# Kernel optimization log

Measured on AMD Instinct MI355X. Metric: run time of the kernel, lower is better.

Reference implementation:

```python
import jax, jax.numpy as jnp
import numpy as np

N = 50000          # nodes
E = 1600000        # edges (avg degree 32)
B = 64             # graphs in batch
IN_CH = 128
HEADS = 8
HD = 8             # head_dim = ceil(64/8)
GH = HEADS * HD    # 64 = gat_hidden_dim
HIDDEN = 64
NC = 10
NEG_SLOPE = 0.2
BN_EPS = 1e-5
SIGMA = 0.5


def setup_inputs() -> dict:
    key = jax.random.key(0)
    ks = jax.random.split(key, 24)
    s = 0.1
    inp = {
        "x": jax.random.normal(ks[0], (N, IN_CH), jnp.float32),
        "raw_x": jax.random.uniform(ks[1], (N, 3), jnp.float32),
        "edge_index": jax.random.randint(ks[2], (2, E), 0, N, jnp.int32),
        "batch": jnp.sort(jax.random.randint(ks[3], (N,), 0, B, jnp.int32)),
        # conv1 (heads=8, out=8, edge_dim=1)
        "W1": jax.random.normal(ks[4], (IN_CH, GH), jnp.float32) * s,
        "att_src1": jax.random.normal(ks[5], (HEADS, HD), jnp.float32) * s,
        "att_dst1": jax.random.normal(ks[6], (HEADS, HD), jnp.float32) * s,
        "We1": jax.random.normal(ks[7], (1, GH), jnp.float32) * s,
        "att_e1": jax.random.normal(ks[8], (HEADS, HD), jnp.float32) * s,
        "b1": jax.random.normal(ks[9], (GH,), jnp.float32) * s,
        "gamma1": jnp.ones((GH,), jnp.float32),
        "beta1": jnp.zeros((GH,), jnp.float32),
        "rm1": jax.random.normal(ks[10], (GH,), jnp.float32) * s,
        "rv1": jax.random.uniform(ks[11], (GH,), jnp.float32) + 0.5,
        # conv2 (heads=1, out=64, edge_dim=1)
        "W2": jax.random.normal(ks[12], (GH, HIDDEN), jnp.float32) * s,
        "att_src2": jax.random.normal(ks[13], (1, HIDDEN), jnp.float32) * s,
        "att_dst2": jax.random.normal(ks[14], (1, HIDDEN), jnp.float32) * s,
        "We2": jax.random.normal(ks[15], (1, HIDDEN), jnp.float32) * s,
        "att_e2": jax.random.normal(ks[16], (1, HIDDEN), jnp.float32) * s,
        "b2": jax.random.normal(ks[17], (HIDDEN,), jnp.float32) * s,
        "gamma2": jnp.ones((HIDDEN,), jnp.float32),
        "beta2": jnp.zeros((HIDDEN,), jnp.float32),
        "rm2": jax.random.normal(ks[18], (HIDDEN,), jnp.float32) * s,
        "rv2": jax.random.uniform(ks[19], (HIDDEN,), jnp.float32) + 0.5,
        # classifier
        "Wc": jax.random.normal(ks[20], (HIDDEN, NC), jnp.float32) * s,
        "bc": jax.random.normal(ks[21], (NC,), jnp.float32) * s,
    }
    return inp


def _gat_conv(x, src, dst, edge_attr, W, a_src, a_dst, W_e, a_e, bias, heads, out_ch, n):
    """PyG GATConv (concat=True, add_self_loops=True, fill_value='mean', eval mode)."""
    e0 = edge_attr.shape[0]
    # self-loop edge_attr = mean of incoming edge_attr per node (0 if isolated)
    cnt = jax.ops.segment_sum(jnp.ones((e0,), x.dtype), dst, num_segments=n)
    loop_attr = jax.ops.segment_sum(edge_attr, dst, num_segments=n) / jnp.maximum(cnt, 1.0)[:, None]
    loops = jnp.arange(n, dtype=src.dtype)
    src2 = jnp.concatenate([src, loops])
    dst2 = jnp.concatenate([dst, loops])
    ea = jnp.concatenate([edge_attr, loop_attr], axis=0)          # [E2, 1]
    h = (x @ W).reshape(n, heads, out_ch)                          # [N, H, D]
    al_s = (h * a_src).sum(-1)                                     # [N, H]
    al_d = (h * a_dst).sum(-1)                                     # [N, H]
    al_e = ((ea @ W_e).reshape(-1, heads, out_ch) * a_e).sum(-1)   # [E2, H]
    logits = al_s[src2] + al_d[dst2] + al_e                        # [E2, H]
    logits = jnp.where(logits >= 0, logits, NEG_SLOPE * logits)    # leaky_relu
    # segment softmax over destination nodes (every node has a self loop)
    m = jax.ops.segment_max(logits, dst2, num_segments=n)
    ex = jnp.exp(logits - m[dst2])
    alpha = ex / jax.ops.segment_sum(ex, dst2, num_segments=n)[dst2]
    out = jax.ops.segment_sum(h[src2] * alpha[:, :, None], dst2, num_segments=n)
    return out.reshape(n, heads * out_ch) + bias


def _bn_eval(x, gamma, beta, rm, rv):
    return (x - rm) * (gamma / jnp.sqrt(rv + BN_EPS)) + beta


def reference(x, raw_x, edge_index, batch,
              W1, att_src1, att_dst1, We1, att_e1, b1, gamma1, beta1, rm1, rv1,
              W2, att_src2, att_dst2, We2, att_e2, b2, gamma2, beta2, rm2, rv2,
              Wc, bc):
    src, dst = edge_index[0], edge_index[1]
    # gaussian edge weights from raw features
    diff = raw_x[src] - raw_x[dst]
    dist2 = (diff * diff).sum(axis=1)
    edge_w = jnp.exp(-dist2 / (2.0 * SIGMA * SIGMA))[:, None]      # [E, 1]
    # eval mode: dropout is identity
    h = _gat_conv(x, src, dst, edge_w, W1, att_src1, att_dst1, We1, att_e1, b1, HEADS, HD, N)
    h = jax.nn.elu(_bn_eval(h, gamma1, beta1, rm1, rv1))
    h = _gat_conv(h, src, dst, edge_w, W2, att_src2, att_dst2, We2, att_e2, b2, 1, HIDDEN, N)
    h = jax.nn.elu(_bn_eval(h, gamma2, beta2, rm2, rv2))
    # global mean pool over graphs
    cnt = jax.ops.segment_sum(jnp.ones((N,), h.dtype), batch, num_segments=B)
    g = jax.ops.segment_sum(h, batch, num_segments=B) / jnp.maximum(cnt, 1.0)[:, None]
    return g @ Wc + bc
```

## Files before the change

kernel.cpp:

```cpp
#include <hip/hip_runtime.h>
#include <math.h>

#define N_NODES 50000
#define N_EDGES 1600000
#define NBATCH  64
#define INCH    128
#define HEADS   8
#define HD      8
#define GH      64
#define HIDDEN  64
#define NC      10
#define NEG_SLOPE 0.2f
#define BN_EPS  1e-5f

#define SCAN_TPB 1024
#define NTILES   ((N_NODES + SCAN_TPB - 1) / SCAN_TPB)

__global__ __launch_bounds__(256) void edge_kernel(
    const int* __restrict__ ei, const float* __restrict__ raw,
    float* __restrict__ ea, float* __restrict__ easum, int* __restrict__ cnt) {
  int e = blockIdx.x * blockDim.x + threadIdx.x;
  if (e >= N_EDGES) return;
  int s = ei[e], d = ei[N_EDGES + e];
  float dx = raw[s*3+0] - raw[d*3+0];
  float dy = raw[s*3+1] - raw[d*3+1];
  float dz = raw[s*3+2] - raw[d*3+2];
  float w = __expf(-2.0f * (dx*dx + dy*dy + dz*dz));
  ea[e] = w;
  atomicAdd(&easum[d], w);
  atomicAdd(&cnt[d], 1);
}

__global__ __launch_bounds__(SCAN_TPB) void scan_part(
    const int* __restrict__ cnt, const float* __restrict__ easum,
    int* __restrict__ rowptr, float* __restrict__ loopat, int* __restrict__ bsum) {
  __shared__ int s[SCAN_TPB];
  int t = threadIdx.x;
  int i = blockIdx.x * SCAN_TPB + t;
  int v = (i < N_NODES) ? cnt[i] : 0;
  s[t] = v; __syncthreads();
  for (int off = 1; off < SCAN_TPB; off <<= 1) {
    int u = (t >= off) ? s[t - off] : 0;
    __syncthreads();
    s[t] += u;
    __syncthreads();
  }
  if (i < N_NODES) {
    rowptr[i] = s[t] - v;
    loopat[i] = easum[i] / fmaxf((float)v, 1.0f);
  }
  if (t == SCAN_TPB - 1) bsum[blockIdx.x] = s[t];
}

__global__ __launch_bounds__(64) void scan_top(int* __restrict__ bsum, int* __restrict__ rowptr) {
  int t = threadIdx.x;
  int v = (t < NTILES) ? bsum[t] : 0;
  int orig = v;
  for (int off = 1; off < 64; off <<= 1) {
    int u = __shfl_up(v, off);
    if (t >= off) v += u;
  }
  if (t < NTILES) bsum[t] = v - orig;
  if (t == 0) rowptr[N_NODES] = N_EDGES;
}

__global__ __launch_bounds__(SCAN_TPB) void scan_add(int* __restrict__ rowptr, const int* __restrict__ bsum) {
  int i = blockIdx.x * SCAN_TPB + threadIdx.x;
  if (i < N_NODES) rowptr[i] += bsum[blockIdx.x];
}

__global__ __launch_bounds__(256) void scatter_kernel(
    const int* __restrict__ ei, const float* __restrict__ ea,
    const int* __restrict__ rowptr, int* __restrict__ cnt2,
    int* __restrict__ csr_src, float* __restrict__ csr_ea) {
  int e = blockIdx.x * blockDim.x + threadIdx.x;
  if (e >= N_EDGES) return;
  int s = ei[e], d = ei[N_EDGES + e];
  int pos = rowptr[d] + atomicAdd(&cnt2[d], 1);
  csr_src[pos] = s;
  csr_ea[pos] = ea[e];
}

__global__ __launch_bounds__(256) void gemm1_kernel(
    const float* __restrict__ x, const float* __restrict__ W1,
    const float* __restrict__ asrc, const float* __restrict__ adst,
    float* __restrict__ h1, float* __restrict__ als, float* __restrict__ ald) {
  __shared__ float w[INCH * GH];
  for (int i = threadIdx.x; i < INCH * GH / 4; i += blockDim.x)
    ((float4*)w)[i] = ((const float4*)W1)[i];
  __syncthreads();
  int lane = threadIdx.x & 63;
  int waveG = __builtin_amdgcn_readfirstlane((blockIdx.x * blockDim.x + threadIdx.x) >> 6);
  int nWaves = (gridDim.x * blockDim.x) >> 6;
  float a_s = asrc[lane];
  float a_d = adst[lane];
  for (int base = waveG * 4; base < N_NODES; base += nWaves * 4) {
    float acc[4] = {0.f, 0.f, 0.f, 0.f};
    #pragma unroll 8
    for (int k = 0; k < INCH; ++k) {
      float wv = w[k * GH + lane];
      #pragma unroll
      for (int j = 0; j < 4; ++j)
        acc[j] = fmaf(x[(size_t)(base + j) * INCH + k], wv, acc[j]);
    }
    #pragma unroll
    for (int j = 0; j < 4; ++j) {
      int n = base + j;
      float hv = acc[j];
      h1[(size_t)n * GH + lane] = hv;
      float ps = hv * a_s, pd = hv * a_d;
      ps += __shfl_xor(ps, 1); ps += __shfl_xor(ps, 2); ps += __shfl_xor(ps, 4);
      pd += __shfl_xor(pd, 1); pd += __shfl_xor(pd, 2); pd += __shfl_xor(pd, 4);
      if ((lane & 7) == 0) {
        als[n * HEADS + (lane >> 3)] = ps;
        ald[n * HEADS + (lane >> 3)] = pd;
      }
    }
  }
}

__global__ __launch_bounds__(256) void conv1_kernel(
    const float* __restrict__ h1, const float* __restrict__ als,
    const float* __restrict__ ald, const float* __restrict__ We,
    const float* __restrict__ ae, const int* __restrict__ rowptr,
    const int* __restrict__ csr_src, const float* __restrict__ csr_ea,
    const float* __restrict__ loopat, const float* __restrict__ bias,
    const float* __restrict__ gamma, const float* __restrict__ beta,
    const float* __restrict__ rm, const float* __restrict__ rv,
    float* __restrict__ h2) {
  int lane = threadIdx.x & 63;
  int n = blockIdx.x * 4 + (threadIdx.x >> 6);
  if (n >= N_NODES) return;
  int h = lane >> 3;
  float ce = 0.f;
  #pragma unroll
  for (int d = 0; d < HD; ++d) ce = fmaf(We[h * HD + d], ae[h * HD + d], ce);
  float aldn = ald[n * HEADS + h];
  int jb = rowptr[n], je = rowptr[n + 1];
  float m = -1e30f, ssum = 0.f, acc = 0.f;
  for (int j = jb; j < je; ++j) {
    int src = csr_src[j];
    float eaj = csr_ea[j];
    float lg = als[src * HEADS + h] + aldn + eaj * ce;
    lg = (lg >= 0.f) ? lg : NEG_SLOPE * lg;
    float hv = h1[(size_t)src * GH + lane];
    float nm = fmaxf(m, lg);
    float r = __expf(m - nm);
    float p = __expf(lg - nm);
    ssum = ssum * r + p;
    acc  = acc  * r + p * hv;
    m = nm;
  }
  {
    float eaj = loopat[n];
    float lg = als[n * HEADS + h] + aldn + eaj * ce;
    lg = (lg >= 0.f) ? lg : NEG_SLOPE * lg;
    float hv = h1[(size_t)n * GH + lane];
    float nm = fmaxf(m, lg);
    float r = __expf(m - nm);
    float p = __expf(lg - nm);
    ssum = ssum * r + p;
    acc  = acc  * r + p * hv;
  }
  float outv = acc / ssum + bias[lane];
  outv = (outv - rm[lane]) * (gamma[lane] * rsqrtf(rv[lane] + BN_EPS)) + beta[lane];
  outv = (outv > 0.f) ? outv : expm1f(outv);
  h2[(size_t)n * GH + lane] = outv;
}

__global__ __launch_bounds__(256) void gemm2_kernel(
    const float* __restrict__ x, const float* __restrict__ W2,
    const float* __restrict__ asrc, const float* __restrict__ adst,
    float* __restrict__ h2m, float* __restrict__ als, float* __restrict__ ald) {
  __shared__ float w[HIDDEN * HIDDEN];
  for (int i = threadIdx.x; i < HIDDEN * HIDDEN / 4; i += blockDim.x)
    ((float4*)w)[i] = ((const float4*)W2)[i];
  __syncthreads();
  int lane = threadIdx.x & 63;
  int waveG = __builtin_amdgcn_readfirstlane((blockIdx.x * blockDim.x + threadIdx.x) >> 6);
  int nWaves = (gridDim.x * blockDim.x) >> 6;
  float a_s = asrc[lane];
  float a_d = adst[lane];
  for (int base = waveG * 4; base < N_NODES; base += nWaves * 4) {
    float acc[4] = {0.f, 0.f, 0.f, 0.f};
    #pragma unroll 8
    for (int k = 0; k < HIDDEN; ++k) {
      float wv = w[k * HIDDEN + lane];
      #pragma unroll
      for (int j = 0; j < 4; ++j)
        acc[j] = fmaf(x[(size_t)(base + j) * HIDDEN + k], wv, acc[j]);
    }
    #pragma unroll
    for (int j = 0; j < 4; ++j) {
      int n = base + j;
      float hv = acc[j];
      h2m[(size_t)n * HIDDEN + lane] = hv;
      float ps = hv * a_s, pd = hv * a_d;
      #pragma unroll
      for (int off = 1; off < 64; off <<= 1) {
        ps += __shfl_xor(ps, off);
        pd += __shfl_xor(pd, off);
      }
      if (lane == 0) { als[n] = ps; ald[n] = pd; }
    }
  }
}

__global__ __launch_bounds__(256) void conv2_kernel(
    const float* __restrict__ h2m, const float* __restrict__ als,
    const float* __restrict__ ald, const float* __restrict__ We,
    const float* __restrict__ ae, const int* __restrict__ rowptr,
    const int* __restrict__ csr_src, const float* __restrict__ csr_ea,
    const float* __restrict__ loopat, const float* __restrict__ bias,
    const float* __restrict__ gamma, const float* __restrict__ beta,
    const float* __restrict__ rm, const float* __restrict__ rv,
    const int* __restrict__ batch,
    float* __restrict__ pool, int* __restrict__ cntg) {
  int lane = threadIdx.x & 63;
  int n = blockIdx.x * 4 + (threadIdx.x >> 6);
  if (n >= N_NODES) return;
  float ce = We[lane] * ae[lane];
  #pragma unroll
  for (int off = 1; off < 64; off <<= 1) ce += __shfl_xor(ce, off);
  float aldn = ald[n];
  int jb = rowptr[n], je = rowptr[n + 1];
  float m = -1e30f, ssum = 0.f, acc = 0.f;
  for (int j = jb; j < je; ++j) {
    int src = csr_src[j];
    float eaj = csr_ea[j];
    float lg = als[src] + aldn + eaj * ce;
    lg = (lg >= 0.f) ? lg : NEG_SLOPE * lg;
    float hv = h2m[(size_t)src * HIDDEN + lane];
    float nm = fmaxf(m, lg);
    float r = __expf(m - nm);
    float p = __expf(lg - nm);
    ssum = ssum * r + p;
    acc  = acc  * r + p * hv;
    m = nm;
  }
  {
    float eaj = loopat[n];
    float lg = als[n] + aldn + eaj * ce;
    lg = (lg >= 0.f) ? lg : NEG_SLOPE * lg;
    float hv = h2m[(size_t)n * HIDDEN + lane];
    float nm = fmaxf(m, lg);
    float r = __expf(m - nm);
    float p = __expf(lg - nm);
    ssum = ssum * r + p;
    acc  = acc  * r + p * hv;
  }
  float outv = acc / ssum + bias[lane];
  outv = (outv - rm[lane]) * (gamma[lane] * rsqrtf(rv[lane] + BN_EPS)) + beta[lane];
  outv = (outv > 0.f) ? outv : expm1f(outv);
  int b = batch[n];
  atomicAdd(&pool[b * HIDDEN + lane], outv);
  if (lane == 0) atomicAdd(&cntg[b], 1);
}

__global__ __launch_bounds__(640) void final_kernel(
    const float* __restrict__ pool, const int* __restrict__ cntg,
    const float* __restrict__ Wc, const float* __restrict__ bc,
    float* __restrict__ out) {
  int t = threadIdx.x;
  if (t >= NBATCH * NC) return;
  int b = t / NC, c = t - b * NC;
  float inv = 1.0f / fmaxf((float)cntg[b], 1.0f);
  float s = bc[c];
  #pragma unroll
  for (int d = 0; d < HIDDEN; ++d)
    s = fmaf(pool[b * HIDDEN + d] * inv, Wc[d * NC + c], s);
  out[t] = s;
}

extern "C" void kernel_launch(void* const* d_in, const int* in_sizes, int n_in,
                              void* d_out, int out_size, void* d_ws, size_t ws_size,
                              hipStream_t stream) {
  const float* x     = (const float*)d_in[0];
  const float* raw   = (const float*)d_in[1];
  const int*   ei    = (const int*)  d_in[2];
  const int*   batch = (const int*)  d_in[3];
  const float* W1    = (const float*)d_in[4];
  const float* asrc1 = (const float*)d_in[5];
  const float* adst1 = (const float*)d_in[6];
  const float* We1   = (const float*)d_in[7];
  const float* ae1   = (const float*)d_in[8];
  const float* b1    = (const float*)d_in[9];
  const float* g1    = (const float*)d_in[10];
  const float* be1   = (const float*)d_in[11];
  const float* rm1   = (const float*)d_in[12];
  const float* rv1   = (const float*)d_in[13];
  const float* W2    = (const float*)d_in[14];
  const float* asrc2 = (const float*)d_in[15];
  const float* adst2 = (const float*)d_in[16];
  const float* We2   = (const float*)d_in[17];
  const float* ae2   = (const float*)d_in[18];
  const float* b2    = (const float*)d_in[19];
  const float* g2    = (const float*)d_in[20];
  const float* be2   = (const float*)d_in[21];
  const float* rm2   = (const float*)d_in[22];
  const float* rv2   = (const float*)d_in[23];
  const float* Wc    = (const float*)d_in[24];
  const float* bc    = (const float*)d_in[25];
  float* out = (float*)d_out;

  char* ws = (char*)d_ws;
  size_t off = 0;
  auto alloc = [&](size_t bytes) -> void* {
    void* p = ws + off;
    off += bytes;
    off = (off + 255) & ~(size_t)255;
    return p;
  };
  float* ea      = (float*)alloc((size_t)N_EDGES * 4);
  float* csr_ea  = (float*)alloc((size_t)N_EDGES * 4);
  int*   csr_src = (int*)  alloc((size_t)N_EDGES * 4);
  float* easum   = (float*)alloc((size_t)N_NODES * 4);
  int*   cnt     = (int*)  alloc((size_t)N_NODES * 4);
  int*   cnt2    = (int*)  alloc((size_t)N_NODES * 4);
  int*   rowptr  = (int*)  alloc((size_t)(N_NODES + 1) * 4);
  float* loopat  = (float*)alloc((size_t)N_NODES * 4);
  float* h1      = (float*)alloc((size_t)N_NODES * GH * 4);
  float* als1    = (float*)alloc((size_t)N_NODES * HEADS * 4);
  float* ald1    = (float*)alloc((size_t)N_NODES * HEADS * 4);
  float* h2      = (float*)alloc((size_t)N_NODES * GH * 4);
  float* h2m     = (float*)alloc((size_t)N_NODES * HIDDEN * 4);
  float* als2    = (float*)alloc((size_t)N_NODES * 4);
  float* ald2    = (float*)alloc((size_t)N_NODES * 4);
  int*   bsum    = (int*)  alloc(64 * 4);
  float* pool    = (float*)alloc((size_t)NBATCH * HIDDEN * 4);
  int*   cntg    = (int*)  alloc((size_t)NBATCH * 4);

  hipMemsetAsync(easum, 0, (size_t)N_NODES * 4, stream);
  hipMemsetAsync(cnt,   0, (size_t)N_NODES * 4, stream);
  hipMemsetAsync(cnt2,  0, (size_t)N_NODES * 4, stream);
  hipMemsetAsync(pool,  0, (size_t)NBATCH * HIDDEN * 4, stream);
  hipMemsetAsync(cntg,  0, (size_t)NBATCH * 4, stream);

  int egrid = (N_EDGES + 255) / 256;
  edge_kernel<<<egrid, 256, 0, stream>>>(ei, raw, ea, easum, cnt);
  scan_part<<<NTILES, SCAN_TPB, 0, stream>>>(cnt, easum, rowptr, loopat, bsum);
  scan_top<<<1, 64, 0, stream>>>(bsum, rowptr);
  scan_add<<<NTILES, SCAN_TPB, 0, stream>>>(rowptr, bsum);
  scatter_kernel<<<egrid, 256, 0, stream>>>(ei, ea, rowptr, cnt2, csr_src, csr_ea);

  gemm1_kernel<<<1024, 256, 0, stream>>>(x, W1, asrc1, adst1, h1, als1, ald1);
  conv1_kernel<<<(N_NODES + 3) / 4, 256, 0, stream>>>(h1, als1, ald1, We1, ae1,
      rowptr, csr_src, csr_ea, loopat, b1, g1, be1, rm1, rv1, h2);
  gemm2_kernel<<<1024, 256, 0, stream>>>(h2, W2, asrc2, adst2, h2m, als2, ald2);
  conv2_kernel<<<(N_NODES + 3) / 4, 256, 0, stream>>>(h2m, als2, ald2, We2, ae2,
      rowptr, csr_src, csr_ea, loopat, b2, g2, be2, rm2, rv2, batch, pool, cntg);
  final_kernel<<<1, 640, 0, stream>>>(pool, cntg, Wc, bc, out);
}
```

Before: 1.067 ms.

## Chunk GAT aggregation: parallel edge logits/softmax per 64-edge chunk, unrolled gathers

Both GAT convolution kernels now process incoming edges in chunks of 64. Source indices and edge attributes are loaded cooperatively across the wave and staged in LDS. Attention logits and the chunk max and sum are computed in parallel with wave shuffles, replacing the per-edge serial online softmax. The feature gather-accumulate is then unrolled by four so several independent row loads are in flight, which removes serial exp and rescale dependencies and scalar index loads per edge. The cost is extra LDS traffic, shuffles and per-chunk padding work for low-degree nodes.

```diff
diff --git a/kernel.cpp b/kernel.cpp
--- a/kernel.cpp
+++ b/kernel.cpp
@@ -128,41 +128,94 @@
     const float* __restrict__ gamma, const float* __restrict__ beta,
     const float* __restrict__ rm, const float* __restrict__ rv,
     float* __restrict__ h2) {
+  __shared__ int   src_lds[4][64];
+  __shared__ float ea_lds[4][64];
+  __shared__ float ex_lds[4][512];
   int lane = threadIdx.x & 63;
-  int n = blockIdx.x * 4 + (threadIdx.x >> 6);
+  int w = threadIdx.x >> 6;
+  int n = blockIdx.x * 4 + w;
   if (n >= N_NODES) return;
-  int h = lane >> 3;
-  float ce = 0.f;
+  int hA = lane & 7;
+  int e8 = lane >> 3;
+  int hB = lane >> 3;
+  float ceA = 0.f;
   #pragma unroll
-  for (int d = 0; d < HD; ++d) ce = fmaf(We[h * HD + d], ae[h * HD + d], ce);
-  float aldn = ald[n * HEADS + h];
+  for (int d = 0; d < HD; ++d) ceA = fmaf(We[hA * HD + d], ae[hA * HD + d], ceA);
+  float aldnA = ald[n * HEADS + hA];
   int jb = rowptr[n], je = rowptr[n + 1];
-  float m = -1e30f, ssum = 0.f, acc = 0.f;
-  for (int j = jb; j < je; ++j) {
-    int src = csr_src[j];
-    float eaj = csr_ea[j];
-    float lg = als[src * HEADS + h] + aldn + eaj * ce;
+  float m = -1e30f, ssum = 0.f;
+  float acc = 0.f;
+  for (int cb = jb; cb < je; cb += 64) {
+    int cnt = je - cb; if (cnt > 64) cnt = 64;
+    int idx = cb + lane;
+    bool vld = lane < cnt;
+    src_lds[w][lane] = vld ? csr_src[idx] : 0;
+    ea_lds[w][lane]  = vld ? csr_ea[idx] : 0.f;
+    float lg[8];
+    #pragma unroll
+    for (int sub = 0; sub < 8; ++sub) {
+      int eo = sub * 8 + e8;
+      int s = src_lds[w][eo];
+      float l = als[s * HEADS + hA] + aldnA + ea_lds[w][eo] * ceA;
+      l = (l >= 0.f) ? l : NEG_SLOPE * l;
+      lg[sub] = (eo < cnt) ? l : -1e30f;
+    }
+    float cm = lg[0];
+    #pragma unroll
+    for (int sub = 1; sub < 8; ++sub) cm = fmaxf(cm, lg[sub]);
+    cm = fmaxf(cm, __shfl_xor(cm, 8));
+    cm = fmaxf(cm, __shfl_xor(cm, 16));
+    cm = fmaxf(cm, __shfl_xor(cm, 32));
+    float nm = fmaxf(m, cm);
+    float sc = __expf(m - nm);
+    float csum = 0.f;
+    #pragma unroll
+    for (int sub = 0; sub < 8; ++sub) {
+      float ex = __expf(lg[sub] - nm);
+      csum += ex;
+      ex_lds[w][sub * 64 + lane] = ex;
+    }
+    csum += __shfl_xor(csum, 8);
+    csum += __shfl_xor(csum, 16);
+    csum += __shfl_xor(csum, 32);
+    ssum = ssum * sc + csum;
+    m = nm;
+    float scB = __shfl(sc, hB);
+    acc *= scB;
+    int j = 0;
+    for (; j + 3 < cnt; j += 4) {
+      int s0 = src_lds[w][j],   s1 = src_lds[w][j+1];
+      int s2 = src_lds[w][j+2], s3 = src_lds[w][j+3];
+      float x0 = ex_lds[w][(j  )*8 + hB], x1 = ex_lds[w][(j+1)*8 + hB];
+      float x2 = ex_lds[w][(j+2)*8 + hB], x3 = ex_lds[w][(j+3)*8 + hB];
+      float v0 = h1[(size_t)s0 * GH + lane];
+      float v1 = h1[(size_t)s1 * GH + lane];
+      float v2 = h1[(size_t)s2 * GH + lane];
+      float v3 = h1[(size_t)s3 * GH + lane];
+      acc = fmaf(x0, v0, acc); acc = fmaf(x1, v1, acc);
+      acc = fmaf(x2, v2, acc); acc = fmaf(x3, v3, acc);
+    }
+    for (; j < cnt; ++j) {
+      int s0 = src_lds[w][j];
+      float x0 = ex_lds[w][j*8 + hB];
+      acc = fmaf(x0, h1[(size_t)s0 * GH + lane], acc);
+    }
+  }
+  float mB = __shfl(m, hB);
+  float sB = __shfl(ssum, hB);
+  float ceB = 0.f;
+  #pragma unroll
+  for (int d = 0; d < HD; ++d) ceB = fmaf(We[hB * HD + d], ae[hB * HD + d], ceB);
+  {
+    float lg = als[n * HEADS + hB] + ald[n * HEADS + hB] + loopat[n] * ceB;
     lg = (lg >= 0.f) ? lg : NEG_SLOPE * lg;
-    float hv = h1[(size_t)src * GH + lane];
-    float nm = fmaxf(m, lg);
-    float r = __expf(m - nm);
+    float nm = fmaxf(mB, lg);
+    float r = __expf(mB - nm);
     float p = __expf(lg - nm);
-    ssum = ssum * r + p;
-    acc  = acc  * r + p * hv;
-    m = nm;
-  }
-  {
-    float eaj = loopat[n];
-    float lg = als[n * HEADS + h] + aldn + eaj * ce;
-    lg = (lg >= 0.f) ? lg : NEG_SLOPE * lg;
-    float hv = h1[(size_t)n * GH + lane];
-    float nm = fmaxf(m, lg);
-    float r = __expf(m - nm);
-    float p = __expf(lg - nm);
-    ssum = ssum * r + p;
-    acc  = acc  * r + p * hv;
-  }
-  float outv = acc / ssum + bias[lane];
+    sB = sB * r + p;
+    acc = acc * r + p * h1[(size_t)n * GH + lane];
+  }
+  float outv = acc / sB + bias[lane];
   outv = (outv - rm[lane]) * (gamma[lane] * rsqrtf(rv[lane] + BN_EPS)) + beta[lane];
   outv = (outv > 0.f) ? outv : expm1f(outv);
   h2[(size_t)n * GH + lane] = outv;
@@ -216,8 +269,11 @@
     const float* __restrict__ rm, const float* __restrict__ rv,
     const int* __restrict__ batch,
     float* __restrict__ pool, int* __restrict__ cntg) {
+  __shared__ int   src_lds[4][64];
+  __shared__ float ex_lds[4][64];
   int lane = threadIdx.x & 63;
-  int n = blockIdx.x * 4 + (threadIdx.x >> 6);
+  int w = threadIdx.x >> 6;
+  int n = blockIdx.x * 4 + w;
   if (n >= N_NODES) return;
   float ce = We[lane] * ae[lane];
   #pragma unroll
@@ -225,29 +281,56 @@
   float aldn = ald[n];
   int jb = rowptr[n], je = rowptr[n + 1];
   float m = -1e30f, ssum = 0.f, acc = 0.f;
-  for (int j = jb; j < je; ++j) {
-    int src = csr_src[j];
-    float eaj = csr_ea[j];
-    float lg = als[src] + aldn + eaj * ce;
+  for (int cb = jb; cb < je; cb += 64) {
+    int cnt = je - cb; if (cnt > 64) cnt = 64;
+    int idx = cb + lane;
+    bool vld = lane < cnt;
+    int sv = vld ? csr_src[idx] : 0;
+    float eav = vld ? csr_ea[idx] : 0.f;
+    src_lds[w][lane] = sv;
+    float lg = als[sv] + aldn + eav * ce;
     lg = (lg >= 0.f) ? lg : NEG_SLOPE * lg;
-    float hv = h2m[(size_t)src * HIDDEN + lane];
+    lg = vld ? lg : -1e30f;
+    float cm = lg;
+    cm = fmaxf(cm, __shfl_xor(cm, 1));  cm = fmaxf(cm, __shfl_xor(cm, 2));
+    cm = fmaxf(cm, __shfl_xor(cm, 4));  cm = fmaxf(cm, __shfl_xor(cm, 8));
+    cm = fmaxf(cm, __shfl_xor(cm, 16)); cm = fmaxf(cm, __shfl_xor(cm, 32));
+    float nm = fmaxf(m, cm);
+    float sc = __expf(m - nm);
+    float ex = __expf(lg - nm);
+    ex_lds[w][lane] = ex;
+    float csum = ex;
+    csum += __shfl_xor(csum, 1);  csum += __shfl_xor(csum, 2);
+    csum += __shfl_xor(csum, 4);  csum += __shfl_xor(csum, 8);
+    csum += __shfl_xor(csum, 16); csum += __shfl_xor(csum, 32);
+    ssum = ssum * sc + csum;
+    m = nm;
+    acc *= sc;
+    int j = 0;
+    for (; j + 3 < cnt; j += 4) {
+      int s0 = src_lds[w][j],   s1 = src_lds[w][j+1];
+      int s2 = src_lds[w][j+2], s3 = src_lds[w][j+3];
+      float x0 = ex_lds[w][j],   x1 = ex_lds[w][j+1];
+      float x2 = ex_lds[w][j+2], x3 = ex_lds[w][j+3];
+      float v0 = h2m[(size_t)s0 * HIDDEN + lane];
+      float v1 = h2m[(size_t)s1 * HIDDEN + lane];
+      float v2 = h2m[(size_t)s2 * HIDDEN + lane];
+      float v3 = h2m[(size_t)s3 * HIDDEN + lane];
+      acc = fmaf(x0, v0, acc); acc = fmaf(x1, v1, acc);
+      acc = fmaf(x2, v2, acc); acc = fmaf(x3, v3, acc);
+    }
+    for (; j < cnt; ++j) {
+      acc = fmaf(ex_lds[w][j], h2m[(size_t)src_lds[w][j] * HIDDEN + lane], acc);
+    }
+  }
+  {
+    float lg = als[n] + aldn + loopat[n] * ce;
+    lg = (lg >= 0.f) ? lg : NEG_SLOPE * lg;
     float nm = fmaxf(m, lg);
     float r = __expf(m - nm);
     float p = __expf(lg - nm);
     ssum = ssum * r + p;
-    acc  = acc  * r + p * hv;
-    m = nm;
-  }
-  {
-    float eaj = loopat[n];
-    float lg = als[n] + aldn + eaj * ce;
-    lg = (lg >= 0.f) ? lg : NEG_SLOPE * lg;
-    float hv = h2m[(size_t)n * HIDDEN + lane];
-    float nm = fmaxf(m, lg);
-    float r = __expf(m - nm);
-    float p = __expf(lg - nm);
-    ssum = ssum * r + p;
-    acc  = acc  * r + p * hv;
+    acc  = acc  * r + p * h2m[(size_t)n * HIDDEN + lane];
   }
   float outv = acc / ssum + bias[lane];
   outv = (outv - rm[lane]) * (gamma[lane] * rsqrtf(rv[lane] + BN_EPS)) + beta[lane];
```

After: 950.9 us. 1.12x faster.

## Store projected features in bf16 and gather four edges per wave in GAT convs

Applied to the files above, without the earlier changes.

The GEMM kernels now write the projected node features as bf16 and no longer compute attention logits. The conv kernels recompute the per-source attention dot product from the gathered bf16 row. Each wave processes four edges at once: 16 lanes per edge, each lane loading 8 bytes. Neighbor indices are staged through LDS, and the next row gather is prefetched. This is meant to halve gather traffic and increase memory-level parallelism in the bandwidth-bound aggregation, at the cost of bf16 rounding in features and logits plus extra shuffle reductions.

```diff
diff --git a/kernel.cpp b/kernel.cpp
--- a/kernel.cpp
+++ b/kernel.cpp
@@ -15,6 +15,18 @@
 
 #define SCAN_TPB 1024
 #define NTILES   ((N_NODES + SCAN_TPB - 1) / SCAN_TPB)
+
+typedef unsigned short ushort_t;
+typedef unsigned int uint_t;
+
+__device__ __forceinline__ ushort_t f2bf(float f) {
+  uint_t u = __float_as_uint(f);
+  uint_t r = (u + 0x7fffu + ((u >> 16) & 1u)) >> 16;
+  return (ushort_t)r;
+}
+__device__ __forceinline__ float2 upk(uint_t u) {
+  return make_float2(__uint_as_float(u << 16), __uint_as_float(u & 0xffff0000u));
+}
 
 __global__ __launch_bounds__(256) void edge_kernel(
     const int* __restrict__ ei, const float* __restrict__ raw,
@@ -83,8 +95,7 @@
 
 __global__ __launch_bounds__(256) void gemm1_kernel(
     const float* __restrict__ x, const float* __restrict__ W1,
-    const float* __restrict__ asrc, const float* __restrict__ adst,
-    float* __restrict__ h1, float* __restrict__ als, float* __restrict__ ald) {
+    ushort_t* __restrict__ h1b) {
   __shared__ float w[INCH * GH];
   for (int i = threadIdx.x; i < INCH * GH / 4; i += blockDim.x)
     ((float4*)w)[i] = ((const float4*)W1)[i];
@@ -92,8 +103,6 @@
   int lane = threadIdx.x & 63;
   int waveG = __builtin_amdgcn_readfirstlane((blockIdx.x * blockDim.x + threadIdx.x) >> 6);
   int nWaves = (gridDim.x * blockDim.x) >> 6;
-  float a_s = asrc[lane];
-  float a_d = adst[lane];
   for (int base = waveG * 4; base < N_NODES; base += nWaves * 4) {
     float acc[4] = {0.f, 0.f, 0.f, 0.f};
     #pragma unroll 8
@@ -104,74 +113,127 @@
         acc[j] = fmaf(x[(size_t)(base + j) * INCH + k], wv, acc[j]);
     }
     #pragma unroll
-    for (int j = 0; j < 4; ++j) {
-      int n = base + j;
-      float hv = acc[j];
-      h1[(size_t)n * GH + lane] = hv;
-      float ps = hv * a_s, pd = hv * a_d;
-      ps += __shfl_xor(ps, 1); ps += __shfl_xor(ps, 2); ps += __shfl_xor(ps, 4);
-      pd += __shfl_xor(pd, 1); pd += __shfl_xor(pd, 2); pd += __shfl_xor(pd, 4);
-      if ((lane & 7) == 0) {
-        als[n * HEADS + (lane >> 3)] = ps;
-        ald[n * HEADS + (lane >> 3)] = pd;
-      }
-    }
+    for (int j = 0; j < 4; ++j)
+      h1b[(size_t)(base + j) * GH + lane] = f2bf(acc[j]);
   }
 }
 
 __global__ __launch_bounds__(256) void conv1_kernel(
-    const float* __restrict__ h1, const float* __restrict__ als,
-    const float* __restrict__ ald, const float* __restrict__ We,
-    const float* __restrict__ ae, const int* __restrict__ rowptr,
+    const ushort_t* __restrict__ h1b,
+    const float* __restrict__ asrc, const float* __restrict__ adst,
+    const float* __restrict__ We, const float* __restrict__ ae,
+    const int* __restrict__ rowptr,
     const int* __restrict__ csr_src, const float* __restrict__ csr_ea,
     const float* __restrict__ loopat, const float* __restrict__ bias,
     const float* __restrict__ gamma, const float* __restrict__ beta,
     const float* __restrict__ rm, const float* __restrict__ rv,
     float* __restrict__ h2) {
-  int lane = threadIdx.x & 63;
-  int n = blockIdx.x * 4 + (threadIdx.x >> 6);
+  __shared__ int   src_lds[4][64];
+  __shared__ float ea_lds[4][64];
+  int l = threadIdx.x & 63;
+  int w = threadIdx.x >> 6;
+  int n = blockIdx.x * 4 + w;
   if (n >= N_NODES) return;
-  int h = lane >> 3;
-  float ce = 0.f;
-  #pragma unroll
-  for (int d = 0; d < HD; ++d) ce = fmaf(We[h * HD + d], ae[h * HD + d], ce);
-  float aldn = ald[n * HEADS + h];
+  int i = l & 15;
+  int q = l >> 4;
+  const float4 as4 = ((const float4*)asrc)[i];
+  const float4 ad4 = ((const float4*)adst)[i];
+  float4 we4 = ((const float4*)We)[i];
+  float4 ae4 = ((const float4*)ae)[i];
+  float ce = we4.x*ae4.x + we4.y*ae4.y + we4.z*ae4.z + we4.w*ae4.w;
+  ce += __shfl_xor(ce, 1);
+  const uint2* tab = (const uint2*)h1b;
+  uint2 uself = tab[(size_t)n * 16 + i];
+  float2 s01 = upk(uself.x), s23 = upk(uself.y);
+  float als_s = s01.x*as4.x + s01.y*as4.y + s23.x*as4.z + s23.y*as4.w;
+  als_s += __shfl_xor(als_s, 1);
+  float aldn  = s01.x*ad4.x + s01.y*ad4.y + s23.x*ad4.z + s23.y*ad4.w;
+  aldn += __shfl_xor(aldn, 1);
   int jb = rowptr[n], je = rowptr[n + 1];
-  float m = -1e30f, ssum = 0.f, acc = 0.f;
-  for (int j = jb; j < je; ++j) {
-    int src = csr_src[j];
-    float eaj = csr_ea[j];
-    float lg = als[src * HEADS + h] + aldn + eaj * ce;
+  float m = -1e30f, ssum = 0.f;
+  float a0 = 0.f, a1 = 0.f, a2 = 0.f, a3 = 0.f;
+  for (int cb = jb; cb < je; cb += 64) {
+    int cnt = je - cb; if (cnt > 64) cnt = 64;
+    int idx = cb + l;
+    bool vld = l < cnt;
+    src_lds[w][l] = vld ? csr_src[idx] : 0;
+    ea_lds[w][l]  = vld ? csr_ea[idx] : 0.f;
+    int nb = (cnt + 3) >> 2;
+    int j0 = q;
+    int s0 = (j0 < cnt) ? src_lds[w][j0] : 0;
+    uint2 rcur = tab[(size_t)s0 * 16 + i];
+    for (int b = 0; b < nb; ++b) {
+      uint2 rnext = rcur;
+      if (b + 1 < nb) {
+        int jn = ((b + 1) << 2) + q;
+        int sn = (jn < cnt) ? src_lds[w][jn] : 0;
+        rnext = tab[(size_t)sn * 16 + i];
+      }
+      int j = (b << 2) + q;
+      bool val = j < cnt;
+      float eav = val ? ea_lds[w][j] : 0.f;
+      float2 p01 = upk(rcur.x), p23 = upk(rcur.y);
+      float dp = p01.x*as4.x + p01.y*as4.y + p23.x*as4.z + p23.y*as4.w;
+      dp += __shfl_xor(dp, 1);
+      float lg = dp + aldn + eav * ce;
+      lg = (lg >= 0.f) ? lg : NEG_SLOPE * lg;
+      lg = val ? lg : -1e30f;
+      float bm = fmaxf(lg, __shfl_xor(lg, 16));
+      bm = fmaxf(bm, __shfl_xor(bm, 32));
+      float nm = fmaxf(m, bm);
+      float sc = __expf(m - nm);
+      float p  = __expf(lg - nm);
+      float ps = p;
+      ps += __shfl_xor(ps, 16);
+      ps += __shfl_xor(ps, 32);
+      ssum = ssum * sc + ps;
+      m = nm;
+      a0 = a0 * sc + p * p01.x;
+      a1 = a1 * sc + p * p01.y;
+      a2 = a2 * sc + p * p23.x;
+      a3 = a3 * sc + p * p23.y;
+      rcur = rnext;
+    }
+  }
+  a0 += __shfl_xor(a0, 16); a0 += __shfl_xor(a0, 32);
+  a1 += __shfl_xor(a1, 16); a1 += __shfl_xor(a1, 32);
+  a2 += __shfl_xor(a2, 16); a2 += __shfl_xor(a2, 32);
+  a3 += __shfl_xor(a3, 16); a3 += __shfl_xor(a3, 32);
+  {
+    float lg = als_s + aldn + loopat[n] * ce;
     lg = (lg >= 0.f) ? lg : NEG_SLOPE * lg;
-    float hv = h1[(size_t)src * GH + lane];
     float nm = fmaxf(m, lg);
-    float r = __expf(m - nm);
-    float p = __expf(lg - nm);
-    ssum = ssum * r + p;
-    acc  = acc  * r + p * hv;
-    m = nm;
-  }
-  {
-    float eaj = loopat[n];
-    float lg = als[n * HEADS + h] + aldn + eaj * ce;
-    lg = (lg >= 0.f) ? lg : NEG_SLOPE * lg;
-    float hv = h1[(size_t)n * GH + lane];
-    float nm = fmaxf(m, lg);
-    float r = __expf(m - nm);
-    float p = __expf(lg - nm);
-    ssum = ssum * r + p;
-    acc  = acc  * r + p * hv;
-  }
-  float outv = acc / ssum + bias[lane];
-  outv = (outv - rm[lane]) * (gamma[lane] * rsqrtf(rv[lane] + BN_EPS)) + beta[lane];
-  outv = (outv > 0.f) ? outv : expm1f(outv);
-  h2[(size_t)n * GH + lane] = outv;
+    float sc = __expf(m - nm);
+    float p  = __expf(lg - nm);
+    ssum = ssum * sc + p;
+    a0 = a0 * sc + p * s01.x;
+    a1 = a1 * sc + p * s01.y;
+    a2 = a2 * sc + p * s23.x;
+    a3 = a3 * sc + p * s23.y;
+  }
+  float inv = 1.0f / ssum;
+  float4 b4 = ((const float4*)bias)[i];
+  float4 g4 = ((const float4*)gamma)[i];
+  float4 be4 = ((const float4*)beta)[i];
+  float4 rm4 = ((const float4*)rm)[i];
+  float4 rv4 = ((const float4*)rv)[i];
+  float o0 = a0 * inv + b4.x, o1 = a1 * inv + b4.y;
+  float o2 = a2 * inv + b4.z, o3 = a3 * inv + b4.w;
+  o0 = (o0 - rm4.x) * (g4.x * rsqrtf(rv4.x + BN_EPS)) + be4.x;
+  o1 = (o1 - rm4.y) * (g4.y * rsqrtf(rv4.y + BN_EPS)) + be4.y;
+  o2 = (o2 - rm4.z) * (g4.z * rsqrtf(rv4.z + BN_EPS)) + be4.z;
+  o3 = (o3 - rm4.w) * (g4.w * rsqrtf(rv4.w + BN_EPS)) + be4.w;
+  o0 = (o0 > 0.f) ? o0 : expm1f(o0);
+  o1 = (o1 > 0.f) ? o1 : expm1f(o1);
+  o2 = (o2 > 0.f) ? o2 : expm1f(o2);
+  o3 = (o3 > 0.f) ? o3 : expm1f(o3);
+  if (q == 0)
+    ((float4*)(h2 + (size_t)n * GH))[i] = make_float4(o0, o1, o2, o3);
 }
 
 __global__ __launch_bounds__(256) void gemm2_kernel(
     const float* __restrict__ x, const float* __restrict__ W2,
-    const float* __restrict__ asrc, const float* __restrict__ adst,
-    float* __restrict__ h2m, float* __restrict__ als, float* __restrict__ ald) {
+    ushort_t* __restrict__ h2mb) {
   __shared__ float w[HIDDEN * HIDDEN];
   for (int i = threadIdx.x; i < HIDDEN * HIDDEN / 4; i += blockDim.x)
     ((float4*)w)[i] = ((const float4*)W2)[i];
@@ -179,8 +241,6 @@
   int lane = threadIdx.x & 63;
   int waveG = __builtin_amdgcn_readfirstlane((blockIdx.x * blockDim.x + threadIdx.x) >> 6);
   int nWaves = (gridDim.x * blockDim.x) >> 6;
-  float a_s = asrc[lane];
-  float a_d = adst[lane];
   for (int base = waveG * 4; base < N_NODES; base += nWaves * 4) {
     float acc[4] = {0.f, 0.f, 0.f, 0.f};
     #pragma unroll 8
@@ -191,70 +251,134 @@
         acc[j] = fmaf(x[(size_t)(base + j) * HIDDEN + k], wv, acc[j]);
     }
     #pragma unroll
-    for (int j = 0; j < 4; ++j) {
-      int n = base + j;
-      float hv = acc[j];
-      h2m[(size_t)n * HIDDEN + lane] = hv;
-      float ps = hv * a_s, pd = hv * a_d;
-      #pragma unroll
-      for (int off = 1; off < 64; off <<= 1) {
-        ps += __shfl_xor(ps, off);
-        pd += __shfl_xor(pd, off);
-      }
-      if (lane == 0) { als[n] = ps; ald[n] = pd; }
-    }
+    for (int j = 0; j < 4; ++j)
+      h2mb[(size_t)(base + j) * HIDDEN + lane] = f2bf(acc[j]);
   }
 }
 
 __global__ __launch_bounds__(256) void conv2_kernel(
-    const float* __restrict__ h2m, const float* __restrict__ als,
-    const float* __restrict__ ald, const float* __restrict__ We,
-    const float* __restrict__ ae, const int* __restrict__ rowptr,
+    const ushort_t* __restrict__ h2mb,
+    const float* __restrict__ asrc, const float* __restrict__ adst,
+    const float* __restrict__ We, const float* __restrict__ ae,
+    const int* __restrict__ rowptr,
     const int* __restrict__ csr_src, const float* __restrict__ csr_ea,
     const float* __restrict__ loopat, const float* __restrict__ bias,
     const float* __restrict__ gamma, const float* __restrict__ beta,
     const float* __restrict__ rm, const float* __restrict__ rv,
     const int* __restrict__ batch,
     float* __restrict__ pool, int* __restrict__ cntg) {
-  int lane = threadIdx.x & 63;
-  int n = blockIdx.x * 4 + (threadIdx.x >> 6);
+  __shared__ int   src_lds[4][64];
+  __shared__ float ea_lds[4][64];
+  int l = threadIdx.x & 63;
+  int w = threadIdx.x >> 6;
+  int n = blockIdx.x * 4 + w;
   if (n >= N_NODES) return;
-  float ce = We[lane] * ae[lane];
-  #pragma unroll
-  for (int off = 1; off < 64; off <<= 1) ce += __shfl_xor(ce, off);
-  float aldn = ald[n];
+  int i = l & 15;
+  int q = l >> 4;
+  const float4 as4 = ((const float4*)asrc)[i];
+  const float4 ad4 = ((const float4*)adst)[i];
+  float4 we4 = ((const float4*)We)[i];
+  float4 ae4 = ((const float4*)ae)[i];
+  float ce = we4.x*ae4.x + we4.y*ae4.y + we4.z*ae4.z + we4.w*ae4.w;
+  ce += __shfl_xor(ce, 1); ce += __shfl_xor(ce, 2);
+  ce += __shfl_xor(ce, 4); ce += __shfl_xor(ce, 8);
+  const uint2* tab = (const uint2*)h2mb;
+  uint2 uself = tab[(size_t)n * 16 + i];
+  float2 s01 = upk(uself.x), s23 = upk(uself.y);
+  float als_s = s01.x*as4.x + s01.y*as4.y + s23.x*as4.z + s23.y*as4.w;
+  als_s += __shfl_xor(als_s, 1); als_s += __shfl_xor(als_s, 2);
+  als_s += __shfl_xor(als_s, 4); als_s += __shfl_xor(als_s, 8);
+  float aldn  = s01.x*ad4.x + s01.y*ad4.y + s23.x*ad4.z + s23.y*ad4.w;
+  aldn += __shfl_xor(aldn, 1); aldn += __shfl_xor(aldn, 2);
+  aldn += __shfl_xor(aldn, 4); aldn += __shfl_xor(aldn, 8);
   int jb = rowptr[n], je = rowptr[n + 1];
-  float m = -1e30f, ssum = 0.f, acc = 0.f;
-  for (int j = jb; j < je; ++j) {
-    int src = csr_src[j];
-    float eaj = csr_ea[j];
-    float lg = als[src] + aldn + eaj * ce;
+  float m = -1e30f, ssum = 0.f;
+  float a0 = 0.f, a1 = 0.f, a2 = 0.f, a3 = 0.f;
+  for (int cb = jb; cb < je; cb += 64) {
+    int cnt = je - cb; if (cnt > 64) cnt = 64;
+    int idx = cb + l;
+    bool vld = l < cnt;
+    src_lds[w][l] = vld ? csr_src[idx] : 0;
+    ea_lds[w][l]  = vld ? csr_ea[idx] : 0.f;
+    int nb = (cnt + 3) >> 2;
+    int j0 = q;
+    int s0 = (j0 < cnt) ? src_lds[w][j0] : 0;
+    uint2 rcur = tab[(size_t)s0 * 16 + i];
+    for (int b = 0; b < nb; ++b) {
+      uint2 rnext = rcur;
+      if (b + 1 < nb) {
+        int jn = ((b + 1) << 2) + q;
+        int sn = (jn < cnt) ? src_lds[w][jn] : 0;
+        rnext = tab[(size_t)sn * 16 + i];
+      }
+      int j = (b << 2) + q;
+      bool val = j < cnt;
+      float eav = val ? ea_lds[w][j] : 0.f;
+      float2 p01 = upk(rcur.x), p23 = upk(rcur.y);
+      float dp = p01.x*as4.x + p01.y*as4.y + p23.x*as4.z + p23.y*as4.w;
+      dp += __shfl_xor(dp, 1); dp += __shfl_xor(dp, 2);
+      dp += __shfl_xor(dp, 4); dp += __shfl_xor(dp, 8);
+      float lg = dp + aldn + eav * ce;
+      lg = (lg >= 0.f) ? lg : NEG_SLOPE * lg;
+      lg = val ? lg : -1e30f;
+      float bm = fmaxf(lg, __shfl_xor(lg, 16));
+      bm = fmaxf(bm, __shfl_xor(bm, 32));
+      float nm = fmaxf(m, bm);
+      float sc = __expf(m - nm);
+      float p  = __expf(lg - nm);
+      float ps = p;
+      ps += __shfl_xor(ps, 16);
+      ps += __shfl_xor(ps, 32);
+      ssum = ssum * sc + ps;
+      m = nm;
+      a0 = a0 * sc + p * p01.x;
+      a1 = a1 * sc + p * p01.y;
+      a2 = a2 * sc + p * p23.x;
+      a3 = a3 * sc + p * p23.y;
+      rcur = rnext;
+    }
+  }
+  a0 += __shfl_xor(a0, 16); a0 += __shfl_xor(a0, 32);
+  a1 += __shfl_xor(a1, 16); a1 += __shfl_xor(a1, 32);
+  a2 += __shfl_xor(a2, 16); a2 += __shfl_xor(a2, 32);
+  a3 += __shfl_xor(a3, 16); a3 += __shfl_xor(a3, 32);
+  {
+    float lg = als_s + aldn + loopat[n] * ce;
     lg = (lg >= 0.f) ? lg : NEG_SLOPE * lg;
-    float hv = h2m[(size_t)src * HIDDEN + lane];
     float nm = fmaxf(m, lg);
-    float r = __expf(m - nm);
-    float p = __expf(lg - nm);
-    ssum = ssum * r + p;
-    acc  = acc  * r + p * hv;
-    m = nm;
-  }
-  {
-    float eaj = loopat[n];
-    float lg = als[n] + aldn + eaj * ce;
-    lg = (lg >= 0.f) ? lg : NEG_SLOPE * lg;
-    float hv = h2m[(size_t)n * HIDDEN + lane];
-    float nm = fmaxf(m, lg);
-    float r = __expf(m - nm);
-    float p = __expf(lg - nm);
-    ssum = ssum * r + p;
-    acc  = acc  * r + p * hv;
-  }
-  float outv = acc / ssum + bias[lane];
-  outv = (outv - rm[lane]) * (gamma[lane] * rsqrtf(rv[lane] + BN_EPS)) + beta[lane];
-  outv = (outv > 0.f) ? outv : expm1f(outv);
-  int b = batch[n];
-  atomicAdd(&pool[b * HIDDEN + lane], outv);
-  if (lane == 0) atomicAdd(&cntg[b], 1);
+    float sc = __expf(m - nm);
+    float p  = __expf(lg - nm);
+    ssum = ssum * sc + p;
+    a0 = a0 * sc + p * s01.x;
+    a1 = a1 * sc + p * s01.y;
+    a2 = a2 * sc + p * s23.x;
+    a3 = a3 * sc + p * s23.y;
+  }
+  float inv = 1.0f / ssum;
+  float4 b4 = ((const float4*)bias)[i];
+  float4 g4 = ((const float4*)gamma)[i];
+  float4 be4 = ((const float4*)beta)[i];
+  float4 rm4 = ((const float4*)rm)[i];
+  float4 rv4 = ((const float4*)rv)[i];
+  float o0 = a0 * inv + b4.x, o1 = a1 * inv + b4.y;
+  float o2 = a2 * inv + b4.z, o3 = a3 * inv + b4.w;
+  o0 = (o0 - rm4.x) * (g4.x * rsqrtf(rv4.x + BN_EPS)) + be4.x;
+  o1 = (o1 - rm4.y) * (g4.y * rsqrtf(rv4.y + BN_EPS)) + be4.y;
+  o2 = (o2 - rm4.z) * (g4.z * rsqrtf(rv4.z + BN_EPS)) + be4.z;
+  o3 = (o3 - rm4.w) * (g4.w * rsqrtf(rv4.w + BN_EPS)) + be4.w;
+  o0 = (o0 > 0.f) ? o0 : expm1f(o0);
+  o1 = (o1 > 0.f) ? o1 : expm1f(o1);
+  o2 = (o2 > 0.f) ? o2 : expm1f(o2);
+  o3 = (o3 > 0.f) ? o3 : expm1f(o3);
+  if (q == 0) {
+    int b = batch[n];
+    float* pp = pool + (size_t)b * HIDDEN + 4 * i;
+    atomicAdd(pp + 0, o0);
+    atomicAdd(pp + 1, o1);
+    atomicAdd(pp + 2, o2);
+    atomicAdd(pp + 3, o3);
+    if (l == 0) atomicAdd(&cntg[b], 1);
+  }
 }
 
 __global__ __launch_bounds__(640) void final_kernel(
@@ -311,24 +435,20 @@
     off = (off + 255) & ~(size_t)255;
     return p;
   };
-  float* ea      = (float*)alloc((size_t)N_EDGES * 4);
-  float* csr_ea  = (float*)alloc((size_t)N_EDGES * 4);
-  int*   csr_src = (int*)  alloc((size_t)N_EDGES * 4);
-  float* easum   = (float*)alloc((size_t)N_NODES * 4);
-  int*   cnt     = (int*)  alloc((size_t)N_NODES * 4);
-  int*   cnt2    = (int*)  alloc((size_t)N_NODES * 4);
-  int*   rowptr  = (int*)  alloc((size_t)(N_NODES + 1) * 4);
-  float* loopat  = (float*)alloc((size_t)N_NODES * 4);
-  float* h1      = (float*)alloc((size_t)N_NODES * GH * 4);
-  float* als1    = (float*)alloc((size_t)N_NODES * HEADS * 4);
-  float* ald1    = (float*)alloc((size_t)N_NODES * HEADS * 4);
-  float* h2      = (float*)alloc((size_t)N_NODES * GH * 4);
-  float* h2m     = (float*)alloc((size_t)N_NODES * HIDDEN * 4);
-  float* als2    = (float*)alloc((size_t)N_NODES * 4);
-  float* ald2    = (float*)alloc((size_t)N_NODES * 4);
-  int*   bsum    = (int*)  alloc(64 * 4);
-  float* pool    = (float*)alloc((size_t)NBATCH * HIDDEN * 4);
-  int*   cntg    = (int*)  alloc((size_t)NBATCH * 4);
+  float*    ea      = (float*)   alloc((size_t)N_EDGES * 4);
+  float*    csr_ea  = (float*)   alloc((size_t)N_EDGES * 4);
+  int*      csr_src = (int*)     alloc((size_t)N_EDGES * 4);
+  float*    easum   = (float*)   alloc((size_t)N_NODES * 4);
+  int*      cnt     = (int*)     alloc((size_t)N_NODES * 4);
+  int*      cnt2    = (int*)     alloc((size_t)N_NODES * 4);
+  int*      rowptr  = (int*)     alloc((size_t)(N_NODES + 1) * 4);
+  float*    loopat  = (float*)   alloc((size_t)N_NODES * 4);
+  ushort_t* h1b     = (ushort_t*)alloc((size_t)N_NODES * GH * 2);
+  float*    h2      = (float*)   alloc((size_t)N_NODES * GH * 4);
+  ushort_t* h2mb    = (ushort_t*)alloc((size_t)N_NODES * HIDDEN * 2);
+  int*      bsum    = (int*)     alloc(64 * 4);
+  float*    pool    = (float*)   alloc((size_t)NBATCH * HIDDEN * 4);
+  int*      cntg    = (int*)     alloc((size_t)NBATCH * 4);
 
   hipMemsetAsync(easum, 0, (size_t)N_NODES * 4, stream);
   hipMemsetAsync(cnt,   0, (size_t)N_NODES * 4, stream);
@@ -343,11 +463,11 @@
   scan_add<<<NTILES, SCAN_TPB, 0, stream>>>(rowptr, bsum);
   scatter_kernel<<<egrid, 256, 0, stream>>>(ei, ea, rowptr, cnt2, csr_src, csr_ea);
 
-  gemm1_kernel<<<1024, 256, 0, stream>>>(x, W1, asrc1, adst1, h1, als1, ald1);
-  conv1_kernel<<<(N_NODES + 3) / 4, 256, 0, stream>>>(h1, als1, ald1, We1, ae1,
+  gemm1_kernel<<<1024, 256, 0, stream>>>(x, W1, h1b);
+  conv1_kernel<<<(N_NODES + 3) / 4, 256, 0, stream>>>(h1b, asrc1, adst1, We1, ae1,
       rowptr, csr_src, csr_ea, loopat, b1, g1, be1, rm1, rv1, h2);
-  gemm2_kernel<<<1024, 256, 0, stream>>>(h2, W2, asrc2, adst2, h2m, als2, ald2);
-  conv2_kernel<<<(N_NODES + 3) / 4, 256, 0, stream>>>(h2m, als2, ald2, We2, ae2,
+  gemm2_kernel<<<1024, 256, 0, stream>>>(h2, W2, h2mb);
+  conv2_kernel<<<(N_NODES + 3) / 4, 256, 0, stream>>>(h2mb, asrc2, adst2, We2, ae2,
       rowptr, csr_src, csr_ea, loopat, b2, g2, be2, rm2, rv2, batch, pool, cntg);
   final_kernel<<<1, 640, 0, stream>>>(pool, cntg, Wc, bc, out);
 }
```

Measured after the change: 929.9 us. 12.8% less time.
